# Optimization experiments

Hardware: AMD Instinct MI355X
Metric: run time of the kernel (lower is better)

Reference implementation:

```python
import jax, jax.numpy as jnp
import numpy as np

B, C, H, W = 8, 512, 64, 64
HEADS = 8
R = 4  # reduction_ratio: depthwise conv kernel=stride=R, padding=R//2
EPS = 1e-5


def _conv(x, w, stride=1, pad=0, groups=1):
    # NCHW / OIHW conv
    return jax.lax.conv_general_dilated(
        x, w, (stride, stride), ((pad, pad), (pad, pad)),
        feature_group_count=groups)


def _layernorm_ch(x, g, b):
    # channel-wise LayerNorm over dim=1 (biased variance, as torch.var(unbiased=False))
    mean = jnp.mean(x, axis=1, keepdims=True)
    var = jnp.var(x, axis=1, keepdims=True)
    return (x - mean) / jnp.sqrt(var + EPS) * g + b


def _to_kv(t, wkv_dw, ln_g, ln_b, wkv_pw):
    t = _conv(t, wkv_dw, stride=R, pad=R // 2, groups=C)  # depthwise strided conv
    t = _layernorm_ch(t, ln_g, ln_b)
    return _conv(t, wkv_pw)  # 1x1 pointwise


def _split_heads(t):
    # 'b (h c) x y -> (b h) (x y) c'
    b, c, x, y = t.shape
    d = c // HEADS
    return t.reshape(b, HEADS, d, x * y).transpose(0, 1, 3, 2).reshape(b * HEADS, x * y, d)


def setup_inputs() -> dict:
    key = jax.random.key(0)
    ks = jax.random.split(key, 7)
    sem = jax.random.normal(ks[0], (B, C, H, W), jnp.float32)
    spa = jax.random.normal(ks[1], (B, C, H, W), jnp.float32)
    x = jax.random.normal(ks[2], (B, C, H, W), jnp.float32)
    wq = jax.random.normal(ks[3], (C, C, 1, 1), jnp.float32) * 0.02
    wkv_dw = jax.random.normal(ks[4], (C, 1, R, R), jnp.float32) * 0.02  # depthwise, groups=C
    ln_g = jnp.ones((1, C, 1, 1), jnp.float32)
    ln_b = jnp.zeros((1, C, 1, 1), jnp.float32)
    wkv_pw = jax.random.normal(ks[5], (C, C, 1, 1), jnp.float32) * 0.02
    wout = jax.random.normal(ks[6], (C, C, 1, 1), jnp.float32) * 0.02
    return {"sem": sem, "spa": spa, "x": x, "wq": wq, "wkv_dw": wkv_dw,
            "ln_g": ln_g, "ln_b": ln_b, "wkv_pw": wkv_pw, "wout": wout}


def reference(sem, spa, x, wq, wkv_dw, ln_g, ln_b, wkv_pw, wout):
    h, w = x.shape[-2:]
    scale = (C // HEADS) ** -0.5
    q = _conv(sem, wq)                               # [B,C,H,W]
    k = _to_kv(spa, wkv_dw, ln_g, ln_b, wkv_pw)      # [B,C,H',W'] downsampled
    v = _to_kv(x, wkv_dw, ln_g, ln_b, wkv_pw)
    q, k, v = map(_split_heads, (q, k, v))           # [(B*h), N, d]
    dots = jnp.einsum('bid,bjd->bij', q, k) * scale  # [(B*h), Nq, Nk]
    attn = jax.nn.softmax(dots, axis=-1)
    out = jnp.einsum('bij,bjd->bid', attn, v)        # [(B*h), Nq, d]
    # '(b h) (x y) c -> b (h c) x y'
    d = C // HEADS
    out = out.reshape(B, HEADS, h * w, d).transpose(0, 1, 3, 2).reshape(B, C, h, w)
    return _conv(out, wout)
```

## Files before the change

kernel.cpp:

```cpp
#include <hip/hip_runtime.h>
#include <hip/hip_bf16.h>


#define BATCH 8
#define CH 512
#define HW 4096
#define NHEADS 8
#define HD 64
#define PP 289
#define NKP 320

typedef __attribute__((ext_vector_type(8))) short bf16x8;
typedef __attribute__((ext_vector_type(4))) float f32x4;

__device__ inline float sanitize(float x) {
    unsigned u = __float_as_uint(x);
    if ((u & 0x7F800000u) == 0x7F800000u) return 0.0f;
    return x;
}
__device__ inline float ldin(const void* p, size_t i, int f32) {
    float x = f32 ? ((const float*)p)[i]
                  : __bfloat162float(((const __hip_bfloat16*)p)[i]);
    return sanitize(x);
}
__device__ inline void stout(void* p, size_t i, float v, int f32) {
    if (f32) ((float*)p)[i] = v;
    else     ((__hip_bfloat16*)p)[i] = __float2bfloat16(v);
}
__device__ inline short f2bf(float x) {
    unsigned u = __float_as_uint(x);
    unsigned r = (u + 0x7FFFu + ((u >> 16) & 1u)) >> 16;
    return (short)r;
}
__device__ inline float bf2f(short s) {
    unsigned u = ((unsigned)(unsigned short)s) << 16;
    return __uint_as_float(u);
}
__device__ inline void gload_lds16(const void* g, void* l) {
    __builtin_amdgcn_global_load_lds(
        (const __attribute__((address_space(1))) void*)g,
        (__attribute__((address_space(3))) void*)l, 16, 0, 0);
}

__global__ void detect_dtype(const unsigned short* __restrict__ w, int* __restrict__ flag) {
    __shared__ int red[256];
    int tid = threadIdx.x;
    int cnt = 0;
    for (int i = tid; i < 8192; i += 256) {
        unsigned e = w[i] & 0x7F80u;
        cnt += (e >= 0x4300u) ? 1 : 0;
    }
    red[tid] = cnt;
    __syncthreads();
    for (int o = 128; o; o >>= 1) { if (tid < o) red[tid] += red[tid + o]; __syncthreads(); }
    if (tid == 0) *flag = (red[0] > 500) ? 1 : 0;
}

__global__ __launch_bounds__(256)
void cvt_w(const void* __restrict__ in, short* __restrict__ out, const int* __restrict__ flag) {
    const int f32 = *flag;
    int i = (blockIdx.x * 256 + threadIdx.x) * 8;
#pragma unroll
    for (int e = 0; e < 8; ++e) out[i + e] = f2bf(ldin(in, i + e, f32));
}

__global__ __launch_bounds__(256)
void wprep(const void* __restrict__ w, const void* __restrict__ g, const void* __restrict__ bb,
           short* __restrict__ wg, float* __restrict__ ws, float* __restrict__ wb,
           const int* __restrict__ flag) {
    const int f32 = *flag;
    const int tid = threadIdx.x;
    const int wave = tid >> 6, lane = tid & 63;
    const int m = blockIdx.x * 4 + wave;
    float s = 0.f, sb = 0.f;
    union { alignas(16) short sh[8]; int4 v; } u;
#pragma unroll
    for (int e = 0; e < 8; ++e) {
        int c = lane * 8 + e;
        float wv = ldin(w, (size_t)m * CH + c, f32);
        float gv = ldin(g, c, f32);
        float bv = ldin(bb, c, f32);
        float p = wv * gv;
        u.sh[e] = f2bf(p);
        s += p;
        sb += wv * bv;
    }
    *(int4*)(wg + (size_t)m * CH + lane * 8) = u.v;
#pragma unroll
    for (int o = 1; o < 64; o <<= 1) {
        s += __shfl_xor(s, o, 64);
        sb += __shfl_xor(sb, o, 64);
    }
    if (lane == 0) { ws[m] = s; wb[m] = sb; }
}

__global__ __launch_bounds__(256)
void transpose_cvt(const void* __restrict__ in, short* __restrict__ outT,
                   const int* __restrict__ flag) {
    __shared__ short T[64 * 72];
    const int f32 = *flag;
    const int tid = threadIdx.x;
    const int z = blockIdx.z;
    const int c0 = blockIdx.y * 64, p0 = blockIdx.x * 64;
    {
        int c = tid >> 2, ps = (tid & 3) * 16;
        size_t src = ((size_t)z * CH + c0 + c) * HW + p0 + ps;
        union { alignas(16) short s[16]; int4 v[2]; } u;
        if (f32) {
            const float4* fp = (const float4*)((const float*)in + src);
#pragma unroll
            for (int v4 = 0; v4 < 4; ++v4) {
                float4 w4 = fp[v4];
                u.s[v4 * 4 + 0] = f2bf(sanitize(w4.x));
                u.s[v4 * 4 + 1] = f2bf(sanitize(w4.y));
                u.s[v4 * 4 + 2] = f2bf(sanitize(w4.z));
                u.s[v4 * 4 + 3] = f2bf(sanitize(w4.w));
            }
        } else {
            const int4* ip = (const int4*)((const short*)in + src);
#pragma unroll
            for (int v4 = 0; v4 < 2; ++v4) {
                union { int4 q; short s[8]; } t; t.q = ip[v4];
#pragma unroll
                for (int e = 0; e < 8; ++e) {
                    short sv = t.s[e];
                    if ((sv & 0x7F80) == 0x7F80) sv = 0;
                    u.s[v4 * 8 + e] = sv;
                }
            }
        }
        int base = c * 144 + ps * 2;
        int k = ((c >> 4) & 3) << 4;
        *(int4*)((char*)T + (base ^ k)) = u.v[0];
        *(int4*)((char*)T + ((base + 16) ^ k)) = u.v[1];
    }
    __syncthreads();
    {
        int p = tid >> 2, cs = (tid & 3) * 16;
        union { short s[16]; int4 v[2]; } u;
#pragma unroll
        for (int e = 0; e < 16; ++e) {
            int row = cs + e;
            int byte = row * 144 + p * 2;
            u.s[e] = *(const short*)((const char*)T + (byte ^ (((row >> 4) & 3) << 4)));
        }
        short* op = outT + ((size_t)z * HW + p0 + p) * CH + c0 + cs;
        *(int4*)op = u.v[0];
        *(int4*)(op + 8) = u.v[1];
    }
}

__global__ __launch_bounds__(256)
void dwconv(const void* __restrict__ in, const void* __restrict__ w,
            float* __restrict__ out, const int* __restrict__ flag) {
    __shared__ float T[4096];
    __shared__ float wf[16];
    const int f32 = *flag;
    const int tid = threadIdx.x;
    const int bc = blockIdx.x;
    const int c = bc & (CH - 1);
    size_t ibase = (size_t)bc * HW;
    if (tid < 16) wf[tid] = ldin(w, (size_t)c * 16 + tid, f32);
    if (f32) {
        const float4* ip = (const float4*)((const float*)in + ibase);
#pragma unroll
        for (int k = 0; k < 4; ++k) {
            float4 v = ip[k * 256 + tid];
            float* d = &T[(k * 256 + tid) * 4];
            d[0] = sanitize(v.x); d[1] = sanitize(v.y);
            d[2] = sanitize(v.z); d[3] = sanitize(v.w);
        }
    } else {
        const int4* ip = (const int4*)((const short*)in + ibase);
#pragma unroll
        for (int k = 0; k < 2; ++k) {
            union { int4 q; unsigned short s[8]; } u; u.q = ip[k * 256 + tid];
            float* d = &T[(k * 256 + tid) * 8];
#pragma unroll
            for (int e = 0; e < 8; ++e) {
                unsigned short sv = u.s[e];
                if ((sv & 0x7F80u) == 0x7F80u) sv = 0;
                d[e] = __bfloat162float(*(__hip_bfloat16*)&sv);
            }
        }
    }
    __syncthreads();
    for (int o = tid; o < PP; o += 256) {
        int oy = o / 17, ox = o % 17;
        float s = 0.f;
#pragma unroll
        for (int ky = 0; ky < 4; ++ky) {
            int iy = oy * 4 - 2 + ky;
            if ((unsigned)iy >= 64u) continue;
#pragma unroll
            for (int kx = 0; kx < 4; ++kx) {
                int ix = ox * 4 - 2 + kx;
                if ((unsigned)ix >= 64u) continue;
                s += T[iy * 64 + ix] * wf[ky * 4 + kx];
            }
        }
        out[(size_t)bc * PP + o] = s;
    }
}

__global__ __launch_bounds__(256)
void transpose_kv(const float* __restrict__ tk, const float* __restrict__ tv,
                  short* __restrict__ tT) {
    __shared__ short T[64 * 72];
    const int tid = threadIdx.x;
    const int zz = blockIdx.z;
    const float* src = (zz < 8 ? tk : tv) + (size_t)(zz & 7) * CH * PP;
    const int c0 = blockIdx.y * 64, p0 = blockIdx.x * 64;
    {
        int c = tid >> 2, ps = (tid & 3) * 16;
        const float* sp = src + (size_t)(c0 + c) * PP + p0 + ps;
        short* dst = &T[c * 72 + ps];
#pragma unroll
        for (int e = 0; e < 16; ++e) {
            int pos = p0 + ps + e;
            dst[e] = (pos < PP) ? f2bf(sp[e]) : (short)0;
        }
    }
    __syncthreads();
    {
        int p = tid >> 2, cs = (tid & 3) * 16;
        union { short s[16]; int4 v[2]; } u;
#pragma unroll
        for (int e = 0; e < 16; ++e) u.s[e] = T[(cs + e) * 72 + p];
        short* op = tT + ((size_t)zz * NKP + p0 + p) * CH + c0 + cs;
        *(int4*)op = u.v[0];
        *(int4*)(op + 8) = u.v[1];
    }
}

__global__ __launch_bounds__(256)
void kv_stats(const short* __restrict__ tT, float* __restrict__ mean,
              float* __restrict__ rstd) {
    const int tid = threadIdx.x;
    const int wave = tid >> 6, lane = tid & 63;
    const int zz = blockIdx.y;
    const int pos = blockIdx.x * 4 + wave;
    bf16x8 v = *(const bf16x8*)(tT + ((size_t)zz * NKP + pos) * CH + lane * 8);
    float s = 0.f, sq = 0.f;
#pragma unroll
    for (int e = 0; e < 8; ++e) {
        float x = bf2f(v[e]);
        s += x; sq += x * x;
    }
#pragma unroll
    for (int o = 1; o < 64; o <<= 1) {
        s += __shfl_xor(s, o, 64);
        sq += __shfl_xor(sq, o, 64);
    }
    if (lane == 0) {
        float m = s * (1.0f / 512.0f);
        float var = sq * (1.0f / 512.0f) - m * m;
        mean[zz * NKP + pos] = m;
        rstd[zz * NKP + pos] = rsqrtf(fmaxf(var, 0.f) + 1e-5f);
    }
}

__global__ __launch_bounds__(256)
void kv_mfma(const short* __restrict__ wg, const short* __restrict__ tT,
             const float* __restrict__ mean, const float* __restrict__ rstd,
             const float* __restrict__ ws, const float* __restrict__ wb,
             short* __restrict__ kpack, short* __restrict__ vpack) {
    __shared__ short Alds[64 * 32];
    __shared__ short Blds[64 * 32];
    const int tid = threadIdx.x;
    const int wave = tid >> 6, lane = tid & 63;
    const int quad = lane >> 4, l15 = lane & 15;
    const int n0 = blockIdx.x * 64, m0 = blockIdx.y * 64;
    const int zz = blockIdx.z;
    const int row = tid >> 2, koff = (tid & 3) * 8;

    f32x4 acc[4];
#pragma unroll
    for (int nf = 0; nf < 4; ++nf) acc[nf] = (f32x4){0.f, 0.f, 0.f, 0.f};

    const short* abase = wg + (size_t)(m0 + row) * CH + koff;
    const short* bbase = tT + ((size_t)zz * NKP + n0 + row) * CH + koff;
    short* al = Alds + row * 32 + koff;
    short* bl = Blds + row * 32 + koff;

    for (int k0 = 0; k0 < CH; k0 += 32) {
        gload_lds16(abase + k0, al);
        gload_lds16(bbase + k0, bl);
        __syncthreads();
        bf16x8 af = *(const bf16x8*)(Alds + (wave * 16 + l15) * 32 + quad * 8);
#pragma unroll
        for (int nf = 0; nf < 4; ++nf) {
            bf16x8 bfr = *(const bf16x8*)(Blds + (nf * 16 + l15) * 32 + quad * 8);
            acc[nf] = __builtin_amdgcn_mfma_f32_16x16x32_bf16(af, bfr, acc[nf], 0, 0, 0);
        }
        __syncthreads();
    }
    const int b = zz & 7;
    const bool isv = zz >= 8;
    float wsv[4], wbv[4];
#pragma unroll
    for (int i = 0; i < 4; ++i) {
        int m = m0 + wave * 16 + quad * 4 + i;
        wsv[i] = ws[m];
        wbv[i] = wb[m];
    }
#pragma unroll
    for (int nf = 0; nf < 4; ++nf) {
        int n = n0 + nf * 16 + l15;
        float mu = mean[zz * NKP + n];
        float rs = rstd[zz * NKP + n];
        bool vld = n < PP;
#pragma unroll
        for (int i = 0; i < 4; ++i) {
            int m = m0 + wave * 16 + quad * 4 + i;
            int head = m >> 6, d = m & 63;
            int bh = b * NHEADS + head;
            float val = vld ? (rs * (acc[nf][i] - mu * wsv[i]) + wbv[i]) : 0.f;
            short sv = f2bf(val);
            if (!isv) kpack[(((size_t)bh * 8 + (d >> 3)) * NKP + n) * 8 + (d & 7)] = sv;
            else      vpack[(((size_t)bh * 40 + (n >> 3)) * HD + d) * 8 + (n & 7)] = sv;
        }
    }
}

__global__ __launch_bounds__(256)
void gemm_mfma(const short* __restrict__ A, const short* __restrict__ Bt,
               void* __restrict__ Cout, const int* __restrict__ flag, int epi) {
    __shared__ short Alds[128 * 32];
    __shared__ short Blds[128 * 32];
    const int f32 = *flag;
    const int tid = threadIdx.x;
    const int wave = tid >> 6, lane = tid & 63;
    const int quad = lane >> 4, l15 = lane & 15;
    const int wm = wave >> 1, wn = wave & 1;
    const int n0 = blockIdx.x * 128, m0 = blockIdx.y * 128;
    const int z = blockIdx.z;
    const int r4 = tid >> 2;
    const int s8 = (tid & 3) * 8;

    f32x4 acc[4][4];
#pragma unroll
    for (int a = 0; a < 4; ++a)
#pragma unroll
        for (int b = 0; b < 4; ++b) acc[a][b] = (f32x4){0.f, 0.f, 0.f, 0.f};

    const short* abase = A + (size_t)(m0 + r4) * 512 + s8;
    const short* bbase = Bt + ((size_t)z * HW + n0 + r4) * 512 + s8;
    short* al = Alds + r4 * 32 + s8;
    short* bl = Blds + r4 * 32 + s8;

    for (int k0 = 0; k0 < 512; k0 += 32) {
#pragma unroll
        for (int c = 0; c < 2; ++c) {
            gload_lds16(abase + (size_t)(c * 64) * 512 + k0, al + c * 2048);
            gload_lds16(bbase + (size_t)(c * 64) * 512 + k0, bl + c * 2048);
        }
        __syncthreads();
        bf16x8 af[4], bfr[4];
#pragma unroll
        for (int a = 0; a < 4; ++a)
            af[a] = *(const bf16x8*)(Alds + (wm * 64 + a * 16 + l15) * 32 + quad * 8);
#pragma unroll
        for (int b = 0; b < 4; ++b)
            bfr[b] = *(const bf16x8*)(Blds + (wn * 64 + b * 16 + l15) * 32 + quad * 8);
#pragma unroll
        for (int a = 0; a < 4; ++a)
#pragma unroll
            for (int b = 0; b < 4; ++b)
                acc[a][b] = __builtin_amdgcn_mfma_f32_16x16x32_bf16(af[a], bfr[b], acc[a][b], 0, 0, 0);
        __syncthreads();
    }
#pragma unroll
    for (int a = 0; a < 4; ++a) {
        int mb = m0 + wm * 64 + a * 16 + quad * 4;
#pragma unroll
        for (int b = 0; b < 4; ++b) {
            int n = n0 + wn * 64 + b * 16 + l15;
            if (epi == 0) {
#pragma unroll
                for (int i = 0; i < 4; ++i)
                    stout(Cout, ((size_t)z * CH + mb + i) * HW + n, acc[a][b][i], f32);
            } else {
                union { alignas(8) short s[4]; int2 v; } u;
#pragma unroll
                for (int i = 0; i < 4; ++i) u.s[i] = f2bf(acc[a][b][i] * 0.18033688011f);
                int h = mb >> 6, d = mb & 63;
                *(int2*)((short*)Cout + ((size_t)(z * NHEADS + h) * HW + n) * HD + d) = u.v;
            }
        }
    }
}

__global__ __launch_bounds__(1024, 1)
void attn_mfma(const short* __restrict__ qt, const short* __restrict__ kpack,
               const short* __restrict__ vpack, short* __restrict__ attT) {
    __shared__ short Klds[8 * NKP * 8];
    __shared__ short Vlds[40 * HD * 8];
    __shared__ short PO[20480];
    const int tid = threadIdx.x;
    const int wave = tid >> 6, lane = tid & 63;
    const int quad = lane >> 4, l15 = lane & 15;
    const int bh = blockIdx.y;
    const int b = bh >> 3, h = bh & 7;

    {
        const short* kbase = kpack + (size_t)bh * (8 * NKP * 8);
        const short* vbase = vpack + (size_t)bh * (40 * HD * 8);
        for (int i = tid; i < 2560; i += 1024) {
            gload_lds16(kbase + i * 8, Klds + i * 8);
            gload_lds16(vbase + i * 8, Vlds + i * 8);
        }
    }
    __syncthreads();

    short* pw = PO + wave * 1280;

    for (int it = 0; it < 2; ++it) {
        const int q0 = blockIdx.x * 1024 + it * 512;
        bf16x8 qf[2][2];
#pragma unroll
        for (int r = 0; r < 2; ++r) {
            const short* qp = qt + ((size_t)bh * HW + q0 + wave * 32 + r * 16 + l15) * HD + quad * 8;
            qf[r][0] = *(const bf16x8*)qp;
            qf[r][1] = *(const bf16x8*)(qp + 32);
        }
        f32x4 O[2][4];
        float lsum[2][4];
#pragma unroll
        for (int r = 0; r < 2; ++r)
#pragma unroll
            for (int df = 0; df < 4; ++df) {
                O[r][df] = (f32x4){0.f, 0.f, 0.f, 0.f};
                lsum[r][df] = 0.f;
            }

#pragma unroll
        for (int sc = 0; sc < 10; ++sc) {
            bf16x8 kf0[2], kf1[2], vf[4];
#pragma unroll
            for (int c2 = 0; c2 < 2; ++c2) {
                const short* kp = Klds + ((size_t)quad * NKP + sc * 32 + c2 * 16 + l15) * 8;
                kf0[c2] = *(const bf16x8*)kp;
                kf1[c2] = *(const bf16x8*)(Klds + ((size_t)(4 + quad) * NKP + sc * 32 + c2 * 16 + l15) * 8);
            }
#pragma unroll
            for (int df = 0; df < 4; ++df)
                vf[df] = *(const bf16x8*)(Vlds + (((size_t)(sc * 4 + quad)) * HD + df * 16 + l15) * 8);
#pragma unroll
            for (int r = 0; r < 2; ++r) {
                short* pwr = pw + r * 640;
#pragma unroll
                for (int c2 = 0; c2 < 2; ++c2) {
                    f32x4 zz = (f32x4){0.f, 0.f, 0.f, 0.f};
                    zz = __builtin_amdgcn_mfma_f32_16x16x32_bf16(qf[r][0], kf0[c2], zz, 0, 0, 0);
                    f32x4 sfv = __builtin_amdgcn_mfma_f32_16x16x32_bf16(qf[r][1], kf1[c2], zz, 0, 0, 0);
#pragma unroll
                    for (int i = 0; i < 4; ++i) {
                        float pv = __builtin_amdgcn_exp2f(fminf(sfv[i], 43.f));
                        lsum[r][i] += pv;
                        pwr[(quad * 4 + i) * 40 + c2 * 16 + l15] = f2bf(pv);
                    }
                }
            }
            asm volatile("s_waitcnt lgkmcnt(0)" ::: "memory");
            __builtin_amdgcn_sched_barrier(0);
            __builtin_amdgcn_s_setprio(1);
#pragma unroll
            for (int r = 0; r < 2; ++r) {
                bf16x8 pf = *(const bf16x8*)(pw + r * 640 + l15 * 40 + quad * 8);
#pragma unroll
                for (int df = 0; df < 4; ++df)
                    O[r][df] = __builtin_amdgcn_mfma_f32_16x16x32_bf16(pf, vf[df], O[r][df], 0, 0, 0);
            }
            __builtin_amdgcn_s_setprio(0);
            asm volatile("" ::: "memory");
        }
#pragma unroll
        for (int r = 0; r < 2; ++r)
#pragma unroll
            for (int i = 0; i < 4; ++i) {
                float s = lsum[r][i];
                s += __shfl_xor(s, 1, 64);
                s += __shfl_xor(s, 2, 64);
                s += __shfl_xor(s, 4, 64);
                s += __shfl_xor(s, 8, 64);
                lsum[r][i] = 1.0f / (s - 31.0f);
            }
        __syncthreads();
#pragma unroll
        for (int hp = 0; hp < 2; ++hp) {
            if ((wave >> 3) == hp) {
                int wl = wave & 7;
#pragma unroll
                for (int r = 0; r < 2; ++r)
#pragma unroll
                    for (int df = 0; df < 4; ++df)
#pragma unroll
                        for (int i = 0; i < 4; ++i)
                            PO[(wl * 32 + r * 16 + quad * 4 + i) * 72 + df * 16 + l15] =
                                f2bf(O[r][df][i] * lsum[r][i]);
            }
            __syncthreads();
            {
                int q = tid >> 2, seg = tid & 3;
                const short* src = PO + q * 72 + seg * 16;
                int4 a0 = *(const int4*)(src);
                int4 a1 = *(const int4*)(src + 8);
                short* op = attT + ((size_t)b * HW + q0 + hp * 256 + q) * CH + h * HD + seg * 16;
                *(int4*)op = a0;
                *(int4*)(op + 8) = a1;
            }
            __syncthreads();
        }
    }
}

extern "C" void kernel_launch(void* const* d_in, const int* in_sizes, int n_in,
                              void* d_out, int out_size, void* d_ws, size_t ws_size,
                              hipStream_t stream) {
    const void* sem    = d_in[0];
    const void* spa    = d_in[1];
    const void* x      = d_in[2];
    const void* wq     = d_in[3];
    const void* wkv_dw = d_in[4];
    const void* ln_g   = d_in[5];
    const void* ln_b   = d_in[6];
    const void* wkv_pw = d_in[7];
    const void* wout   = d_in[8];

    const size_t nkv = (size_t)BATCH * CH * PP;
    char* p = (char*)d_ws;
    auto alloc = [&](size_t bytes) { char* r = p; p += (bytes + 255) & ~(size_t)255; return r; };
    int*   flag  = (int*)alloc(256);
    float* tk    = (float*)alloc(nkv * 4);
    float* tv    = (float*)alloc(nkv * 4);
    short* kpk   = (short*)alloc((size_t)64 * 8 * NKP * 8 * 2);
    short* vpk   = (short*)alloc((size_t)64 * 40 * HD * 8 * 2);
    short* semT  = (short*)alloc((size_t)BATCH * HW * CH * 2);
    short* attT  = (short*)alloc((size_t)BATCH * HW * CH * 2);
    short* wqb   = (short*)alloc((size_t)512 * 512 * 2);
    short* woutb = (short*)alloc((size_t)512 * 512 * 2);
    short* qt    = (short*)d_out;

    short* tT    = (short*)d_out;
    short* wg    = attT;
    float* ws    = (float*)(attT + (size_t)512 * 512);
    float* wb    = ws + 512;
    float* meanp = wb + 512;
    float* rstdp = meanp + 16 * NKP;

    detect_dtype<<<1, 256, 0, stream>>>((const unsigned short*)sem, flag);

    cvt_w<<<128, 256, 0, stream>>>(wq, wqb, flag);
    cvt_w<<<128, 256, 0, stream>>>(wout, woutb, flag);
    wprep<<<128, 256, 0, stream>>>(wkv_pw, ln_g, ln_b, wg, ws, wb, flag);

    dim3 gt(HW / 64, CH / 64, BATCH);
    transpose_cvt<<<gt, 256, 0, stream>>>(sem, semT, flag);

    dwconv<<<BATCH * CH, 256, 0, stream>>>(spa, wkv_dw, tk, flag);
    dwconv<<<BATCH * CH, 256, 0, stream>>>(x,   wkv_dw, tv, flag);

    dim3 gtk(NKP / 64, CH / 64, 16);
    transpose_kv<<<gtk, 256, 0, stream>>>(tk, tv, tT);

    dim3 gs(NKP / 4, 16);
    kv_stats<<<gs, 256, 0, stream>>>(tT, meanp, rstdp);

    dim3 gkv(NKP / 64, CH / 64, 16);
    kv_mfma<<<gkv, 256, 0, stream>>>(wg, tT, meanp, rstdp, ws, wb, kpk, vpk);

    dim3 gg(HW / 128, CH / 128, BATCH);
    gemm_mfma<<<gg, 256, 0, stream>>>(wqb, semT, qt, flag, 1);

    dim3 ga(HW / 1024, 64);
    attn_mfma<<<ga, 1024, 0, stream>>>(qt, kpk, vpk, attT);

    gemm_mfma<<<gg, 256, 0, stream>>>(woutb, attT, d_out, flag, 0);
}
```

Baseline: 395.7 us.

## Split attention into smaller per-block query tiles and read V from global

Restructures the attention kernel so each 1024-thread block handles 256 queries (one 16-row tile per wave) instead of 1024 queries over two iterations, which quadruples the grid. V fragments are now loaded directly from global memory instead of being staged in LDS, and the P/O scratch buffers are shrunk. This is meant to raise occupancy and parallelism and cut LDS footprint. In exchange, K is loaded into LDS four times as often, V is read from global repeatedly, and per-wave MFMA work is halved. The launch bound hint changes to 8 blocks per CU, which is unachievable for 1024-thread blocks.

Result: slower. 416.0 us (+5.1%).

```diff
diff --git a/kernel.cpp b/kernel.cpp
--- a/kernel.cpp
+++ b/kernel.cpp
@@ -391,127 +391,99 @@
     }
 }
 
-__global__ __launch_bounds__(1024, 1)
+__global__ __launch_bounds__(1024, 8)
 void attn_mfma(const short* __restrict__ qt, const short* __restrict__ kpack,
                const short* __restrict__ vpack, short* __restrict__ attT) {
     __shared__ short Klds[8 * NKP * 8];
-    __shared__ short Vlds[40 * HD * 8];
-    __shared__ short PO[20480];
+    __shared__ short PO[18432];
     const int tid = threadIdx.x;
     const int wave = tid >> 6, lane = tid & 63;
     const int quad = lane >> 4, l15 = lane & 15;
     const int bh = blockIdx.y;
     const int b = bh >> 3, h = bh & 7;
+    const int q0 = blockIdx.x * 256;
 
     {
         const short* kbase = kpack + (size_t)bh * (8 * NKP * 8);
-        const short* vbase = vpack + (size_t)bh * (40 * HD * 8);
-        for (int i = tid; i < 2560; i += 1024) {
+        for (int i = tid; i < 2560; i += 1024)
             gload_lds16(kbase + i * 8, Klds + i * 8);
-            gload_lds16(vbase + i * 8, Vlds + i * 8);
-        }
-    }
-    __syncthreads();
-
-    short* pw = PO + wave * 1280;
-
-    for (int it = 0; it < 2; ++it) {
-        const int q0 = blockIdx.x * 1024 + it * 512;
-        bf16x8 qf[2][2];
-#pragma unroll
-        for (int r = 0; r < 2; ++r) {
-            const short* qp = qt + ((size_t)bh * HW + q0 + wave * 32 + r * 16 + l15) * HD + quad * 8;
-            qf[r][0] = *(const bf16x8*)qp;
-            qf[r][1] = *(const bf16x8*)(qp + 32);
-        }
-        f32x4 O[2][4];
-        float lsum[2][4];
-#pragma unroll
-        for (int r = 0; r < 2; ++r)
-#pragma unroll
-            for (int df = 0; df < 4; ++df) {
-                O[r][df] = (f32x4){0.f, 0.f, 0.f, 0.f};
-                lsum[r][df] = 0.f;
+    }
+
+    bf16x8 qf0, qf1;
+    {
+        const short* qp = qt + ((size_t)bh * HW + q0 + wave * 16 + l15) * HD + quad * 8;
+        qf0 = *(const bf16x8*)qp;
+        qf1 = *(const bf16x8*)(qp + 32);
+    }
+    const short* vbase = vpack + (size_t)bh * (40 * HD * 8);
+
+    f32x4 O[4];
+    float lsum[4] = {0.f, 0.f, 0.f, 0.f};
+#pragma unroll
+    for (int df = 0; df < 4; ++df) O[df] = (f32x4){0.f, 0.f, 0.f, 0.f};
+    short* pw = PO + wave * 576;
+    __syncthreads();
+
+#pragma unroll
+    for (int sc = 0; sc < 10; ++sc) {
+        bf16x8 vf[4];
+#pragma unroll
+        for (int df = 0; df < 4; ++df)
+            vf[df] = *(const bf16x8*)(vbase + (((size_t)(sc * 4 + quad)) * HD + df * 16 + l15) * 8);
+        bf16x8 kf0[2], kf1[2];
+#pragma unroll
+        for (int c2 = 0; c2 < 2; ++c2) {
+            kf0[c2] = *(const bf16x8*)(Klds + ((size_t)quad * NKP + sc * 32 + c2 * 16 + l15) * 8);
+            kf1[c2] = *(const bf16x8*)(Klds + ((size_t)(4 + quad) * NKP + sc * 32 + c2 * 16 + l15) * 8);
+        }
+#pragma unroll
+        for (int c2 = 0; c2 < 2; ++c2) {
+            f32x4 zz = (f32x4){0.f, 0.f, 0.f, 0.f};
+            zz = __builtin_amdgcn_mfma_f32_16x16x32_bf16(qf0, kf0[c2], zz, 0, 0, 0);
+            f32x4 sfv = __builtin_amdgcn_mfma_f32_16x16x32_bf16(qf1, kf1[c2], zz, 0, 0, 0);
+#pragma unroll
+            for (int i = 0; i < 4; ++i) {
+                float pv = __builtin_amdgcn_exp2f(fminf(sfv[i], 43.f));
+                lsum[i] += pv;
+                pw[(quad * 4 + i) * 36 + c2 * 16 + l15] = f2bf(pv);
             }
-
-#pragma unroll
-        for (int sc = 0; sc < 10; ++sc) {
-            bf16x8 kf0[2], kf1[2], vf[4];
-#pragma unroll
-            for (int c2 = 0; c2 < 2; ++c2) {
-                const short* kp = Klds + ((size_t)quad * NKP + sc * 32 + c2 * 16 + l15) * 8;
-                kf0[c2] = *(const bf16x8*)kp;
-                kf1[c2] = *(const bf16x8*)(Klds + ((size_t)(4 + quad) * NKP + sc * 32 + c2 * 16 + l15) * 8);
-            }
+        }
+        asm volatile("s_waitcnt lgkmcnt(0)" ::: "memory");
+        __builtin_amdgcn_sched_barrier(0);
+        __builtin_amdgcn_s_setprio(1);
+        {
+            bf16x8 pf = *(const bf16x8*)(pw + l15 * 36 + quad * 8);
 #pragma unroll
             for (int df = 0; df < 4; ++df)
-                vf[df] = *(const bf16x8*)(Vlds + (((size_t)(sc * 4 + quad)) * HD + df * 16 + l15) * 8);
-#pragma unroll
-            for (int r = 0; r < 2; ++r) {
-                short* pwr = pw + r * 640;
-#pragma unroll
-                for (int c2 = 0; c2 < 2; ++c2) {
-                    f32x4 zz = (f32x4){0.f, 0.f, 0.f, 0.f};
-                    zz = __builtin_amdgcn_mfma_f32_16x16x32_bf16(qf[r][0], kf0[c2], zz, 0, 0, 0);
-                    f32x4 sfv = __builtin_amdgcn_mfma_f32_16x16x32_bf16(qf[r][1], kf1[c2], zz, 0, 0, 0);
-#pragma unroll
-                    for (int i = 0; i < 4; ++i) {
-                        float pv = __builtin_amdgcn_exp2f(fminf(sfv[i], 43.f));
-                        lsum[r][i] += pv;
-                        pwr[(quad * 4 + i) * 40 + c2 * 16 + l15] = f2bf(pv);
-                    }
-                }
-            }
-            asm volatile("s_waitcnt lgkmcnt(0)" ::: "memory");
-            __builtin_amdgcn_sched_barrier(0);
-            __builtin_amdgcn_s_setprio(1);
-#pragma unroll
-            for (int r = 0; r < 2; ++r) {
-                bf16x8 pf = *(const bf16x8*)(pw + r * 640 + l15 * 40 + quad * 8);
-#pragma unroll
-                for (int df = 0; df < 4; ++df)
-                    O[r][df] = __builtin_amdgcn_mfma_f32_16x16x32_bf16(pf, vf[df], O[r][df], 0, 0, 0);
-            }
-            __builtin_amdgcn_s_setprio(0);
-            asm volatile("" ::: "memory");
-        }
-#pragma unroll
-        for (int r = 0; r < 2; ++r)
-#pragma unroll
-            for (int i = 0; i < 4; ++i) {
-                float s = lsum[r][i];
-                s += __shfl_xor(s, 1, 64);
-                s += __shfl_xor(s, 2, 64);
-                s += __shfl_xor(s, 4, 64);
-                s += __shfl_xor(s, 8, 64);
-                lsum[r][i] = 1.0f / (s - 31.0f);
-            }
-        __syncthreads();
-#pragma unroll
-        for (int hp = 0; hp < 2; ++hp) {
-            if ((wave >> 3) == hp) {
-                int wl = wave & 7;
-#pragma unroll
-                for (int r = 0; r < 2; ++r)
-#pragma unroll
-                    for (int df = 0; df < 4; ++df)
-#pragma unroll
-                        for (int i = 0; i < 4; ++i)
-                            PO[(wl * 32 + r * 16 + quad * 4 + i) * 72 + df * 16 + l15] =
-                                f2bf(O[r][df][i] * lsum[r][i]);
-            }
-            __syncthreads();
-            {
-                int q = tid >> 2, seg = tid & 3;
-                const short* src = PO + q * 72 + seg * 16;
-                int4 a0 = *(const int4*)(src);
-                int4 a1 = *(const int4*)(src + 8);
-                short* op = attT + ((size_t)b * HW + q0 + hp * 256 + q) * CH + h * HD + seg * 16;
-                *(int4*)op = a0;
-                *(int4*)(op + 8) = a1;
-            }
-            __syncthreads();
-        }
+                O[df] = __builtin_amdgcn_mfma_f32_16x16x32_bf16(pf, vf[df], O[df], 0, 0, 0);
+        }
+        __builtin_amdgcn_s_setprio(0);
+        asm volatile("" ::: "memory");
+    }
+#pragma unroll
+    for (int i = 0; i < 4; ++i) {
+        float s = lsum[i];
+        s += __shfl_xor(s, 1, 64);
+        s += __shfl_xor(s, 2, 64);
+        s += __shfl_xor(s, 4, 64);
+        s += __shfl_xor(s, 8, 64);
+        lsum[i] = 1.0f / (s - 31.0f);
+    }
+    __syncthreads();
+#pragma unroll
+    for (int df = 0; df < 4; ++df)
+#pragma unroll
+        for (int i = 0; i < 4; ++i)
+            PO[(wave * 16 + quad * 4 + i) * 72 + df * 16 + l15] = f2bf(O[df][i] * lsum[i]);
+    __syncthreads();
+    {
+        int q = tid >> 2, seg = tid & 3;
+        const short* src = PO + q * 72 + seg * 16;
+        int4 a0 = *(const int4*)(src);
+        int4 a1 = *(const int4*)(src + 8);
+        short* op = attT + ((size_t)b * HW + q0 + q) * CH + h * HD + seg * 16;
+        *(int4*)op = a0;
+        *(int4*)(op + 8) = a1;
     }
 }
 
@@ -573,7 +545,7 @@
     dim3 gg(HW / 128, CH / 128, BATCH);
     gemm_mfma<<<gg, 256, 0, stream>>>(wqb, semT, qt, flag, 1);
 
-    dim3 ga(HW / 1024, 64);
+    dim3 ga(HW / 256, 64);
     attn_mfma<<<ga, 1024, 0, stream>>>(qt, kpk, vpk, attT);
 
     gemm_mfma<<<gg, 256, 0, stream>>>(woutb, attT, d_out, flag, 0);
```
